# Kernel optimization log

Measured on AMD Instinct MI355X. Metric: run time of the kernel, lower is better.

The kernel has to match this reference:

```python
import jax, jax.numpy as jnp
import numpy as np

N_NODES = 50000

def gcn_conv(x, src, dst, W, b, n_nodes):
    """PyG-style GCNConv: add self-loops, symmetric norm, linear (no bias in lin),
    scatter-add aggregation, then bias."""
    loops = jnp.arange(n_nodes, dtype=src.dtype)
    s = jnp.concatenate([src, loops])  # [E+N]
    d = jnp.concatenate([dst, loops])  # [E+N]
    # degree on destination (col) with unit edge weights, incl. self loops
    deg = jax.ops.segment_sum(jnp.ones_like(d, dtype=x.dtype), d, num_segments=n_nodes)
    dinv = jnp.where(deg > 0, jax.lax.rsqrt(jnp.maximum(deg, 1.0)), 0.0)
    norm = dinv[s] * dinv[d]  # [E+N]
    h = x @ W  # [N, out]
    msg = h[s] * norm[:, None]  # [E+N, out] gather + scale
    out = jax.ops.segment_sum(msg, d, num_segments=n_nodes)  # scatter-add
    return out + b

def setup_inputs() -> dict:
    key = jax.random.key(0)
    k1, k2, k3, k4, k5, k6 = jax.random.split(key, 6)
    n, d_in, h_dim, d_out, e = N_NODES, 128, 128, 64, 800000
    x = jax.random.normal(k1, (n, d_in), dtype=jnp.float32)
    src = jax.random.randint(k2, (e,), 0, n, dtype=jnp.int64)
    dst = jax.random.randint(k3, (e,), 0, n, dtype=jnp.int64)
    edge_index = jnp.stack([src, dst])
    # Glorot-ish init for weights, zeros for bias (PyG default)
    W1 = jax.random.normal(k4, (d_in, h_dim), dtype=jnp.float32) / np.sqrt(d_in)
    b1 = jnp.zeros((h_dim,), dtype=jnp.float32)
    W2 = jax.random.normal(k5, (h_dim, d_out), dtype=jnp.float32) / np.sqrt(h_dim)
    b2 = jnp.zeros((d_out,), dtype=jnp.float32)
    return {"x": x, "edge_index": edge_index, "W1": W1, "b1": b1, "W2": W2, "b2": b2}

def reference(x, edge_index, W1, b1, W2, b2):
    src, dst = edge_index[0], edge_index[1]
    n = x.shape[0]
    h = gcn_conv(x, src, dst, W1, b1, n)
    h = jax.nn.relu(h)
    out = gcn_conv(h, src, dst, W2, b2, n)
    return jax.nn.relu(out)
```

## Files before the change

### kernel.cpp

```cpp
#include <hip/hip_runtime.h>


#define NPB 64
#define PB  256

typedef unsigned short ushort_t;
typedef unsigned int uint_t;
typedef __attribute__((ext_vector_type(8))) short bf16x8;
typedef __attribute__((ext_vector_type(4))) float f32x4;

__device__ inline float bf2f_lo(uint_t u) { return __uint_as_float(u << 16); }
__device__ inline float bf2f_hi(uint_t u) { return __uint_as_float(u & 0xffff0000u); }
__device__ inline ushort_t f2bf(float f) {
    uint_t x = __float_as_uint(f);
    uint_t r = x + 0x7fffu + ((x >> 16) & 1u);
    return (ushort_t)(r >> 16);
}
__device__ inline uint_t pack2bf(float lo, float hi) {
    return (uint_t)f2bf(lo) | ((uint_t)f2bf(hi) << 16);
}

__global__ __launch_bounds__(256) void prep_w_kernel(const float* __restrict__ W1,
                                                     const float* __restrict__ W2,
                                                     ushort_t* __restrict__ W1f,
                                                     ushort_t* __restrict__ W2f) {
    int i = blockIdx.x * 256 + threadIdx.x;
    if (i < 128 * 128) {
        int k = i >> 7, c = i & 127;
        int ct = c >> 4, lo = c & 15, ks = k >> 5, kg = (k >> 3) & 3, j = k & 7;
        W1f[(size_t)(((ct * 4 + ks) * 64) + kg * 16 + lo) * 8 + j] = f2bf(W1[i]);
    }
    if (i < 128 * 64) {
        int k = i >> 6, c = i & 63;
        int ct = c >> 4, lo = c & 15, ks = k >> 5, kg = (k >> 3) & 3, j = k & 7;
        W2f[(size_t)(((ct * 4 + ks) * 64) + kg * 16 + lo) * 8 + j] = f2bf(W2[i]);
    }
}


__global__ __launch_bounds__(256) void block_sum_kernel(const int* __restrict__ a, int L,
                                                        int* __restrict__ bsum) {
    __shared__ int red[256];
    int t = threadIdx.x;
    int base = blockIdx.x * 1024 + t * 4;
    int s = 0;
    if (base + 3 < L) {
        int4 v = *(const int4*)&a[base];
        s = v.x + v.y + v.z + v.w;
    } else {
        for (int i = 0; i < 4; ++i) if (base + i < L) s += a[base + i];
    }
    red[t] = s;
    __syncthreads();
    for (int off = 128; off > 0; off >>= 1) {
        if (t < off) red[t] += red[t + off];
        __syncthreads();
    }
    if (t == 0) bsum[blockIdx.x] = red[0];
}

__global__ __launch_bounds__(256) void local_scan_apply_kernel(int* __restrict__ arr, int L,
                                                               const int* __restrict__ bsum,
                                                               int nb) {
    __shared__ int sh[256];
    __shared__ int tsum[256];
    int b = blockIdx.x, t = threadIdx.x;
    sh[t] = (t < nb) ? bsum[t] : 0;
    __syncthreads();
    #pragma unroll
    for (int off = 1; off < 256; off <<= 1) {
        int w = (t >= off) ? sh[t - off] : 0;
        __syncthreads();
        sh[t] += w;
        __syncthreads();
    }
    int bprev = (b == 0) ? 0 : sh[b - 1];

    int base = b * 1024 + t * 4;
    int v[4];
    int s = 0;
    #pragma unroll
    for (int i = 0; i < 4; ++i) {
        int idx = base + i;
        v[i] = (idx < L) ? arr[idx] : 0;
        s += v[i];
    }
    tsum[t] = s;
    __syncthreads();
    for (int off = 1; off < 256; off <<= 1) {
        int w = (t >= off) ? tsum[t - off] : 0;
        __syncthreads();
        tsum[t] += w;
        __syncthreads();
    }
    int excl = (t == 0 ? 0 : tsum[t - 1]) + bprev;
    #pragma unroll
    for (int i = 0; i < 4; ++i) {
        int idx = base + i;
        if (idx < L) {
            arr[idx] = excl;
            excl += v[i];
        }
    }
}

__global__ __launch_bounds__(256) void local_scan_node_kernel(const int* __restrict__ cnt, int n,
                                                              const int* __restrict__ bsum,
                                                              int nb, int e_total,
                                                              int* __restrict__ rowstart,
                                                              float* __restrict__ dinv) {
    __shared__ int sh[256];
    __shared__ int tsum[256];
    int b = blockIdx.x, t = threadIdx.x;
    sh[t] = (t < nb) ? bsum[t] : 0;
    __syncthreads();
    #pragma unroll
    for (int off = 1; off < 256; off <<= 1) {
        int w = (t >= off) ? sh[t - off] : 0;
        __syncthreads();
        sh[t] += w;
        __syncthreads();
    }
    int bprev = (b == 0) ? 0 : sh[b - 1];

    int base = b * 1024 + t * 4;
    int v[4];
    int s = 0;
    #pragma unroll
    for (int i = 0; i < 4; ++i) {
        int idx = base + i;
        v[i] = (idx < n) ? cnt[idx] : 0;
        s += v[i];
    }
    tsum[t] = s;
    __syncthreads();
    for (int off = 1; off < 256; off <<= 1) {
        int w = (t >= off) ? tsum[t - off] : 0;
        __syncthreads();
        tsum[t] += w;
        __syncthreads();
    }
    int excl = (t == 0 ? 0 : tsum[t - 1]) + bprev;
    #pragma unroll
    for (int i = 0; i < 4; ++i) {
        int idx = base + i;
        if (idx < n) {
            rowstart[idx] = excl;
            excl += v[i];
            dinv[idx] = rsqrtf((float)(v[i] + 1));
        }
    }
    if (b == 0 && t == 0) rowstart[n] = e_total;
}


__global__ __launch_bounds__(256) void bucket_hist_kernel(const int* __restrict__ dst, int e,
                                                          int epb, int K,
                                                          int* __restrict__ hist) {
    __shared__ int lh[1024];
    int t = threadIdx.x, b = blockIdx.x;
    for (int k = t; k < K; k += 256) lh[k] = 0;
    __syncthreads();
    int lo = b * epb, hi = min(lo + epb, e);
    for (int i = lo + t; i < hi; i += 256) atomicAdd(&lh[dst[i] >> 6], 1);
    __syncthreads();
    for (int k = t; k < K; k += 256) hist[k * PB + b] = lh[k];
}

__global__ __launch_bounds__(256) void partition_kernel(const int* __restrict__ src,
                                                        const int* __restrict__ dst, int e,
                                                        int epb, int K,
                                                        const int* __restrict__ hist,
                                                        uint_t* __restrict__ ebuf) {
    __shared__ int loff[1024];
    int t = threadIdx.x, b = blockIdx.x;
    for (int k = t; k < K; k += 256) loff[k] = hist[k * PB + b];
    __syncthreads();
    int lo = b * epb, hi = min(lo + epb, e);
    for (int i = lo + t; i < hi; i += 256) {
        int d = dst[i];
        int k = d >> 6;
        int pos = atomicAdd(&loff[k], 1);
        ebuf[pos] = (uint_t)src[i] | ((uint_t)(d & (NPB - 1)) << 16);
    }
}

__global__ __launch_bounds__(256) void bucket_count_kernel(const uint_t* __restrict__ ebuf,
                                                           const int* __restrict__ hist,
                                                           int e, int K, int n,
                                                           int* __restrict__ cnt) {
    __shared__ int c64[NPB];
    int t = threadIdx.x, k = blockIdx.x;
    if (t < NPB) c64[t] = 0;
    __syncthreads();
    int lo = hist[k * PB];
    int hi = (k + 1 < K) ? hist[(k + 1) * PB] : e;
    for (int i = lo + t; i < hi; i += 256) atomicAdd(&c64[(ebuf[i] >> 16) & (NPB - 1)], 1);
    __syncthreads();
    int node = k * NPB + t;
    if (t < NPB && node < n) cnt[node] = c64[t];
}

__global__ __launch_bounds__(256) void bucket_fill_kernel(const uint_t* __restrict__ ebuf,
                                                          const int* __restrict__ hist,
                                                          const int* __restrict__ rowstart,
                                                          int e, int K, int n,
                                                          ushort_t* __restrict__ csr_src) {
    __shared__ int rs[NPB];
    __shared__ int c64[NPB];
    int t = threadIdx.x, k = blockIdx.x;
    if (t < NPB) {
        int node = k * NPB + t;
        rs[t] = (node < n) ? rowstart[node] : 0;
        c64[t] = 0;
    }
    __syncthreads();
    int lo = hist[k * PB];
    int hi = (k + 1 < K) ? hist[(k + 1) * PB] : e;
    for (int i = lo + t; i < hi; i += 256) {
        uint_t u = __builtin_nontemporal_load(ebuf + i);
        int dl = (u >> 16) & (NPB - 1);
        int slot = rs[dl] + atomicAdd(&c64[dl], 1);
        csr_src[slot] = (ushort_t)(u & 0xffffu);
    }
}

__global__ __launch_bounds__(256) void gemm128_mfma_kernel(const float* __restrict__ A,
                                                           const ushort_t* __restrict__ Wf,
                                                           const float* __restrict__ dinv,
                                                           ushort_t* __restrict__ out, int n) {
    __shared__ ushort_t Asl[64][136];
    int t = threadIdx.x;
    int row0 = blockIdx.x * 64;

    #pragma unroll
    for (int it = 0; it < 4; ++it) {
        int idx = (it * 256 + t) * 8;
        int r = idx >> 7, k = idx & 127;
        int gr = row0 + r;
        uint4 p = {0u, 0u, 0u, 0u};
        if (gr < n) {
            float4 lo = *(const float4*)&A[(size_t)gr * 128 + k];
            float4 hi = *(const float4*)&A[(size_t)gr * 128 + k + 4];
            p.x = pack2bf(lo.x, lo.y); p.y = pack2bf(lo.z, lo.w);
            p.z = pack2bf(hi.x, hi.y); p.w = pack2bf(hi.z, hi.w);
        }
        *(uint4*)&Asl[r][k] = p;
    }
    __syncthreads();

    int wave = t >> 6, lane = t & 63;
    int rb = wave * 16;
    int lrow = rb + (lane & 15);
    int kg8 = (lane >> 4) * 8;

    bf16x8 a0 = *(const bf16x8*)&Asl[lrow][0 * 32 + kg8];
    bf16x8 a1 = *(const bf16x8*)&Asl[lrow][1 * 32 + kg8];
    bf16x8 a2 = *(const bf16x8*)&Asl[lrow][2 * 32 + kg8];
    bf16x8 a3 = *(const bf16x8*)&Asl[lrow][3 * 32 + kg8];

    f32x4 acc[8];
    #pragma unroll
    for (int ct = 0; ct < 8; ++ct) acc[ct] = (f32x4){0.f, 0.f, 0.f, 0.f};

    #pragma unroll
    for (int ct = 0; ct < 8; ++ct) {
        const bf16x8* Wp = (const bf16x8*)&Wf[(size_t)(ct * 4) * 64 * 8];
        bf16x8 b0 = Wp[0 * 64 + lane];
        bf16x8 b1 = Wp[1 * 64 + lane];
        bf16x8 b2 = Wp[2 * 64 + lane];
        bf16x8 b3 = Wp[3 * 64 + lane];
        acc[ct] = __builtin_amdgcn_mfma_f32_16x16x32_bf16(a0, b0, acc[ct], 0, 0, 0);
        acc[ct] = __builtin_amdgcn_mfma_f32_16x16x32_bf16(a1, b1, acc[ct], 0, 0, 0);
        acc[ct] = __builtin_amdgcn_mfma_f32_16x16x32_bf16(a2, b2, acc[ct], 0, 0, 0);
        acc[ct] = __builtin_amdgcn_mfma_f32_16x16x32_bf16(a3, b3, acc[ct], 0, 0, 0);
    }

    int orow0 = row0 + rb + (lane >> 4) * 4;
    int col0 = lane & 15;
    float dv[4];
    #pragma unroll
    for (int r = 0; r < 4; ++r) dv[r] = (orow0 + r < n) ? dinv[orow0 + r] : 0.f;
    #pragma unroll
    for (int ct = 0; ct < 8; ++ct) {
        #pragma unroll
        for (int r = 0; r < 4; ++r) {
            int row = orow0 + r;
            if (row < n) out[(size_t)row * 128 + ct * 16 + col0] = f2bf(acc[ct][r] * dv[r]);
        }
    }
}

__global__ __launch_bounds__(256) void gemm64_mfma_kernel(const ushort_t* __restrict__ A,
                                                          const ushort_t* __restrict__ Wf,
                                                          const float* __restrict__ dinv,
                                                          ushort_t* __restrict__ out, int n) {
    __shared__ ushort_t Asl[64][136];
    int t = threadIdx.x;
    int row0 = blockIdx.x * 64;

    #pragma unroll
    for (int it = 0; it < 4; ++it) {
        int idx = (it * 256 + t) * 8;
        int r = idx >> 7, k = idx & 127;
        int gr = row0 + r;
        uint4 p = {0u, 0u, 0u, 0u};
        if (gr < n) p = *(const uint4*)&A[(size_t)gr * 128 + k];
        *(uint4*)&Asl[r][k] = p;
    }
    __syncthreads();

    int wave = t >> 6, lane = t & 63;
    int rb = wave * 16;
    int lrow = rb + (lane & 15);
    int kg8 = (lane >> 4) * 8;

    bf16x8 a0 = *(const bf16x8*)&Asl[lrow][0 * 32 + kg8];
    bf16x8 a1 = *(const bf16x8*)&Asl[lrow][1 * 32 + kg8];
    bf16x8 a2 = *(const bf16x8*)&Asl[lrow][2 * 32 + kg8];
    bf16x8 a3 = *(const bf16x8*)&Asl[lrow][3 * 32 + kg8];

    f32x4 acc[4];
    #pragma unroll
    for (int ct = 0; ct < 4; ++ct) acc[ct] = (f32x4){0.f, 0.f, 0.f, 0.f};

    #pragma unroll
    for (int ct = 0; ct < 4; ++ct) {
        const bf16x8* Wp = (const bf16x8*)&Wf[(size_t)(ct * 4) * 64 * 8];
        bf16x8 b0 = Wp[0 * 64 + lane];
        bf16x8 b1 = Wp[1 * 64 + lane];
        bf16x8 b2 = Wp[2 * 64 + lane];
        bf16x8 b3 = Wp[3 * 64 + lane];
        acc[ct] = __builtin_amdgcn_mfma_f32_16x16x32_bf16(a0, b0, acc[ct], 0, 0, 0);
        acc[ct] = __builtin_amdgcn_mfma_f32_16x16x32_bf16(a1, b1, acc[ct], 0, 0, 0);
        acc[ct] = __builtin_amdgcn_mfma_f32_16x16x32_bf16(a2, b2, acc[ct], 0, 0, 0);
        acc[ct] = __builtin_amdgcn_mfma_f32_16x16x32_bf16(a3, b3, acc[ct], 0, 0, 0);
    }

    int orow0 = row0 + rb + (lane >> 4) * 4;
    int col0 = lane & 15;
    float dv[4];
    #pragma unroll
    for (int r = 0; r < 4; ++r) dv[r] = (orow0 + r < n) ? dinv[orow0 + r] : 0.f;
    #pragma unroll
    for (int ct = 0; ct < 4; ++ct) {
        #pragma unroll
        for (int r = 0; r < 4; ++r) {
            int row = orow0 + r;
            if (row < n) out[(size_t)row * 64 + ct * 16 + col0] = f2bf(acc[ct][r] * dv[r]);
        }
    }
}

__global__ __launch_bounds__(256) void aggregate128_kernel(const ushort_t* __restrict__ g,
                                                           const int* __restrict__ rowstart,
                                                           const ushort_t* __restrict__ csr_src,
                                                           const float* __restrict__ dinv,
                                                           const float* __restrict__ bias,
                                                           ushort_t* __restrict__ out, int n) {
    int wave = threadIdx.x >> 6;
    int lane = threadIdx.x & 63;
    int v = blockIdx.x * 4 + wave;
    if (v >= n) return;
    int s    = __builtin_amdgcn_readfirstlane(rowstart[v]);
    int epos = __builtin_amdgcn_readfirstlane(rowstart[v + 1]);
    int eg = lane >> 3;
    int f  = lane & 7;

    float a0 = 0.f, a1 = 0.f, a2 = 0.f, a3 = 0.f, a4 = 0.f, a5 = 0.f, a6 = 0.f, a7 = 0.f;
    float a8 = 0.f, a9 = 0.f, aA = 0.f, aB = 0.f, aC = 0.f, aD = 0.f, aE = 0.f, aF = 0.f;
    if (lane < 8) {
        uint4 m0 = *(const uint4*)&g[(size_t)v * 128 + f * 16];
        uint4 m1 = *(const uint4*)&g[(size_t)v * 128 + f * 16 + 8];
        a0 = bf2f_lo(m0.x); a1 = bf2f_hi(m0.x);
        a2 = bf2f_lo(m0.y); a3 = bf2f_hi(m0.y);
        a4 = bf2f_lo(m0.z); a5 = bf2f_hi(m0.z);
        a6 = bf2f_lo(m0.w); a7 = bf2f_hi(m0.w);
        a8 = bf2f_lo(m1.x); a9 = bf2f_hi(m1.x);
        aA = bf2f_lo(m1.y); aB = bf2f_hi(m1.y);
        aC = bf2f_lo(m1.z); aD = bf2f_hi(m1.z);
        aE = bf2f_lo(m1.w); aF = bf2f_hi(m1.w);
    }

    #pragma unroll 2
    for (int j = s; j < epos; j += 8) {
        int idx = j + eg;
        int safe = min(idx, epos - 1);
        int u = csr_src[safe];
        float w = (idx < epos) ? 1.f : 0.f;
        uint4 m0 = *(const uint4*)&g[(size_t)u * 128 + f * 16];
        uint4 m1 = *(const uint4*)&g[(size_t)u * 128 + f * 16 + 8];
        a0 = fmaf(w, bf2f_lo(m0.x), a0); a1 = fmaf(w, bf2f_hi(m0.x), a1);
        a2 = fmaf(w, bf2f_lo(m0.y), a2); a3 = fmaf(w, bf2f_hi(m0.y), a3);
        a4 = fmaf(w, bf2f_lo(m0.z), a4); a5 = fmaf(w, bf2f_hi(m0.z), a5);
        a6 = fmaf(w, bf2f_lo(m0.w), a6); a7 = fmaf(w, bf2f_hi(m0.w), a7);
        a8 = fmaf(w, bf2f_lo(m1.x), a8); a9 = fmaf(w, bf2f_hi(m1.x), a9);
        aA = fmaf(w, bf2f_lo(m1.y), aA); aB = fmaf(w, bf2f_hi(m1.y), aB);
        aC = fmaf(w, bf2f_lo(m1.z), aC); aD = fmaf(w, bf2f_hi(m1.z), aD);
        aE = fmaf(w, bf2f_lo(m1.w), aE); aF = fmaf(w, bf2f_hi(m1.w), aF);
    }

    #pragma unroll
    for (int m = 8; m <= 32; m <<= 1) {
        a0 += __shfl_xor(a0, m); a1 += __shfl_xor(a1, m);
        a2 += __shfl_xor(a2, m); a3 += __shfl_xor(a3, m);
        a4 += __shfl_xor(a4, m); a5 += __shfl_xor(a5, m);
        a6 += __shfl_xor(a6, m); a7 += __shfl_xor(a7, m);
        a8 += __shfl_xor(a8, m); a9 += __shfl_xor(a9, m);
        aA += __shfl_xor(aA, m); aB += __shfl_xor(aB, m);
        aC += __shfl_xor(aC, m); aD += __shfl_xor(aD, m);
        aE += __shfl_xor(aE, m); aF += __shfl_xor(aF, m);
    }

    if (lane < 8) {
        float dv = dinv[v];
        int c0 = f * 16;
        float4 b0 = *(const float4*)&bias[c0];
        float4 b1 = *(const float4*)&bias[c0 + 4];
        float4 b2 = *(const float4*)&bias[c0 + 8];
        float4 b3 = *(const float4*)&bias[c0 + 12];
        float o00 = fmaxf(fmaf(a0, dv, b0.x), 0.f), o01 = fmaxf(fmaf(a1, dv, b0.y), 0.f);
        float o02 = fmaxf(fmaf(a2, dv, b0.z), 0.f), o03 = fmaxf(fmaf(a3, dv, b0.w), 0.f);
        float o04 = fmaxf(fmaf(a4, dv, b1.x), 0.f), o05 = fmaxf(fmaf(a5, dv, b1.y), 0.f);
        float o06 = fmaxf(fmaf(a6, dv, b1.z), 0.f), o07 = fmaxf(fmaf(a7, dv, b1.w), 0.f);
        float o08 = fmaxf(fmaf(a8, dv, b2.x), 0.f), o09 = fmaxf(fmaf(a9, dv, b2.y), 0.f);
        float o10 = fmaxf(fmaf(aA, dv, b2.z), 0.f), o11 = fmaxf(fmaf(aB, dv, b2.w), 0.f);
        float o12 = fmaxf(fmaf(aC, dv, b3.x), 0.f), o13 = fmaxf(fmaf(aD, dv, b3.y), 0.f);
        float o14 = fmaxf(fmaf(aE, dv, b3.z), 0.f), o15 = fmaxf(fmaf(aF, dv, b3.w), 0.f);
        uint4 p0 = {pack2bf(o00, o01), pack2bf(o02, o03), pack2bf(o04, o05), pack2bf(o06, o07)};
        uint4 p1 = {pack2bf(o08, o09), pack2bf(o10, o11), pack2bf(o12, o13), pack2bf(o14, o15)};
        *(uint4*)&out[(size_t)v * 128 + c0]     = p0;
        *(uint4*)&out[(size_t)v * 128 + c0 + 8] = p1;
    }
}

__global__ __launch_bounds__(256) void aggregate64_kernel(const ushort_t* __restrict__ g,
                                                          const int* __restrict__ rowstart,
                                                          const ushort_t* __restrict__ csr_src,
                                                          const float* __restrict__ dinv,
                                                          const float* __restrict__ bias,
                                                          float* __restrict__ out, int n) {
    int wave = threadIdx.x >> 6;
    int lane = threadIdx.x & 63;
    int v = blockIdx.x * 4 + wave;
    if (v >= n) return;
    int s    = __builtin_amdgcn_readfirstlane(rowstart[v]);
    int epos = __builtin_amdgcn_readfirstlane(rowstart[v + 1]);
    int eg = lane >> 3;
    int f  = lane & 7;

    float a0 = 0.f, a1 = 0.f, a2 = 0.f, a3 = 0.f, a4 = 0.f, a5 = 0.f, a6 = 0.f, a7 = 0.f;
    if (lane < 8) {
        uint4 m = *(const uint4*)&g[(size_t)v * 64 + f * 8];
        a0 = bf2f_lo(m.x); a1 = bf2f_hi(m.x);
        a2 = bf2f_lo(m.y); a3 = bf2f_hi(m.y);
        a4 = bf2f_lo(m.z); a5 = bf2f_hi(m.z);
        a6 = bf2f_lo(m.w); a7 = bf2f_hi(m.w);
    }

    #pragma unroll 2
    for (int j = s; j < epos; j += 8) {
        int idx = j + eg;
        int safe = min(idx, epos - 1);
        int u = __builtin_nontemporal_load(csr_src + safe);
        float w = (idx < epos) ? 1.f : 0.f;
        uint4 m = *(const uint4*)&g[(size_t)u * 64 + f * 8];
        a0 = fmaf(w, bf2f_lo(m.x), a0); a1 = fmaf(w, bf2f_hi(m.x), a1);
        a2 = fmaf(w, bf2f_lo(m.y), a2); a3 = fmaf(w, bf2f_hi(m.y), a3);
        a4 = fmaf(w, bf2f_lo(m.z), a4); a5 = fmaf(w, bf2f_hi(m.z), a5);
        a6 = fmaf(w, bf2f_lo(m.w), a6); a7 = fmaf(w, bf2f_hi(m.w), a7);
    }

    a0 += __shfl_xor(a0, 8);  a1 += __shfl_xor(a1, 8);
    a2 += __shfl_xor(a2, 8);  a3 += __shfl_xor(a3, 8);
    a4 += __shfl_xor(a4, 8);  a5 += __shfl_xor(a5, 8);
    a6 += __shfl_xor(a6, 8);  a7 += __shfl_xor(a7, 8);
    a0 += __shfl_xor(a0, 16); a1 += __shfl_xor(a1, 16);
    a2 += __shfl_xor(a2, 16); a3 += __shfl_xor(a3, 16);
    a4 += __shfl_xor(a4, 16); a5 += __shfl_xor(a5, 16);
    a6 += __shfl_xor(a6, 16); a7 += __shfl_xor(a7, 16);
    a0 += __shfl_xor(a0, 32); a1 += __shfl_xor(a1, 32);
    a2 += __shfl_xor(a2, 32); a3 += __shfl_xor(a3, 32);
    a4 += __shfl_xor(a4, 32); a5 += __shfl_xor(a5, 32);
    a6 += __shfl_xor(a6, 32); a7 += __shfl_xor(a7, 32);

    if (lane < 8) {
        float dv = dinv[v];
        float4 b0 = *(const float4*)&bias[f * 8];
        float4 b1 = *(const float4*)&bias[f * 8 + 4];
        float4 o0 = {fmaxf(fmaf(a0, dv, b0.x), 0.f), fmaxf(fmaf(a1, dv, b0.y), 0.f),
                     fmaxf(fmaf(a2, dv, b0.z), 0.f), fmaxf(fmaf(a3, dv, b0.w), 0.f)};
        float4 o1 = {fmaxf(fmaf(a4, dv, b1.x), 0.f), fmaxf(fmaf(a5, dv, b1.y), 0.f),
                     fmaxf(fmaf(a6, dv, b1.z), 0.f), fmaxf(fmaf(a7, dv, b1.w), 0.f)};
        *(float4*)&out[(size_t)v * 64 + f * 8] = o0;
        *(float4*)&out[(size_t)v * 64 + f * 8 + 4] = o1;
    }
}

extern "C" void kernel_launch(void* const* d_in, const int* in_sizes, int n_in,
                              void* d_out, int out_size, void* d_ws, size_t ws_size,
                              hipStream_t stream) {
    const float* x  = (const float*)d_in[0];
    const int*   ei = (const int*)d_in[1];
    const float* W1 = (const float*)d_in[2];
    const float* b1 = (const float*)d_in[3];
    const float* W2 = (const float*)d_in[4];
    const float* b2 = (const float*)d_in[5];
    float* out = (float*)d_out;

    const int n = in_sizes[0] / 128;
    const int e = in_sizes[1] / 2;
    const int* src = ei;
    const int* dst = ei + e;
    const int K   = (n + NPB - 1) / NPB;
    const int epb = (e + PB - 1) / PB;
    const int L   = K * PB;

    char* ws = (char*)d_ws;
    size_t off = 0;
    auto carve = [&](size_t bytes) -> void* {
        void* p = ws + off;
        off = (off + bytes + 255) & ~(size_t)255;
        return p;
    };
    int*      hist     = (int*)     carve((size_t)L * 4);
    int*      bsum     = (int*)     carve((size_t)1024 * 4);
    int*      cnt      = (int*)     carve((size_t)n * 4);
    int*      rowstart = (int*)     carve((size_t)(n + 1) * 4);
    float*    dinv     = (float*)   carve((size_t)n * 4);
    uint_t*   ebuf     = (uint_t*)  carve((size_t)e * 4);
    ushort_t* csr_src  = (ushort_t*)carve((size_t)e * 2);
    ushort_t* W1f      = (ushort_t*)carve((size_t)128 * 128 * 2);
    ushort_t* W2f      = (ushort_t*)carve((size_t)128 * 64 * 2);
    ushort_t* g1       = (ushort_t*)carve((size_t)n * 128 * 2);
    ushort_t* h2       = (ushort_t*)carve((size_t)n * 128 * 2);
    ushort_t* g2       = (ushort_t*)carve((size_t)n * 64 * 2);
    (void)ws_size;

    const int nbL = (L + 1023) / 1024;
    const int nbN = (n + 1023) / 1024;

    prep_w_kernel<<<64, 256, 0, stream>>>(W1, W2, W1f, W2f);
    bucket_hist_kernel<<<PB, 256, 0, stream>>>(dst, e, epb, K, hist);
    block_sum_kernel<<<nbL, 256, 0, stream>>>(hist, L, bsum);
    local_scan_apply_kernel<<<nbL, 256, 0, stream>>>(hist, L, bsum, nbL);
    partition_kernel<<<PB, 256, 0, stream>>>(src, dst, e, epb, K, hist, ebuf);
    bucket_count_kernel<<<K, 256, 0, stream>>>(ebuf, hist, e, K, n, cnt);
    block_sum_kernel<<<nbN, 256, 0, stream>>>(cnt, n, bsum);
    local_scan_node_kernel<<<nbN, 256, 0, stream>>>(cnt, n, bsum, nbN, e, rowstart, dinv);
    bucket_fill_kernel<<<K, 256, 0, stream>>>(ebuf, hist, rowstart, e, K, n, csr_src);

    const int gblocks = (n + 63) / 64;
    const int ablocks = (n + 3) / 4;
    gemm128_mfma_kernel<<<gblocks, 256, 0, stream>>>(x, W1f, dinv, g1, n);
    aggregate128_kernel<<<ablocks, 256, 0, stream>>>(g1, rowstart, csr_src, dinv, b1, h2, n);
    gemm64_mfma_kernel<<<gblocks, 256, 0, stream>>>(h2, W2f, dinv, g2, n);
    aggregate64_kernel<<<ablocks, 256, 0, stream>>>(g2, rowstart, csr_src, dinv, b2, out, n);
}
```

Baseline: 130.3 us.

## Fuse layer-1 aggregation with layer-2 GEMM and merge prep kernels

```diff
diff --git a/kernel.cpp b/kernel.cpp
--- a/kernel.cpp
+++ b/kernel.cpp
@@ -18,23 +18,6 @@
 }
 __device__ inline uint_t pack2bf(float lo, float hi) {
     return (uint_t)f2bf(lo) | ((uint_t)f2bf(hi) << 16);
-}
-
-__global__ __launch_bounds__(256) void prep_w_kernel(const float* __restrict__ W1,
-                                                     const float* __restrict__ W2,
-                                                     ushort_t* __restrict__ W1f,
-                                                     ushort_t* __restrict__ W2f) {
-    int i = blockIdx.x * 256 + threadIdx.x;
-    if (i < 128 * 128) {
-        int k = i >> 7, c = i & 127;
-        int ct = c >> 4, lo = c & 15, ks = k >> 5, kg = (k >> 3) & 3, j = k & 7;
-        W1f[(size_t)(((ct * 4 + ks) * 64) + kg * 16 + lo) * 8 + j] = f2bf(W1[i]);
-    }
-    if (i < 128 * 64) {
-        int k = i >> 6, c = i & 63;
-        int ct = c >> 4, lo = c & 15, ks = k >> 5, kg = (k >> 3) & 3, j = k & 7;
-        W2f[(size_t)(((ct * 4 + ks) * 64) + kg * 16 + lo) * 8 + j] = f2bf(W2[i]);
-    }
 }
 
 
@@ -105,23 +88,13 @@
 }
 
 __global__ __launch_bounds__(256) void local_scan_node_kernel(const int* __restrict__ cnt, int n,
-                                                              const int* __restrict__ bsum,
-                                                              int nb, int e_total,
+                                                              const int* __restrict__ hist,
+                                                              int e_total,
                                                               int* __restrict__ rowstart,
                                                               float* __restrict__ dinv) {
-    __shared__ int sh[256];
     __shared__ int tsum[256];
     int b = blockIdx.x, t = threadIdx.x;
-    sh[t] = (t < nb) ? bsum[t] : 0;
-    __syncthreads();
-    #pragma unroll
-    for (int off = 1; off < 256; off <<= 1) {
-        int w = (t >= off) ? sh[t - off] : 0;
-        __syncthreads();
-        sh[t] += w;
-        __syncthreads();
-    }
-    int bprev = (b == 0) ? 0 : sh[b - 1];
+    int bprev = hist[(size_t)(b * 16) * PB];
 
     int base = b * 1024 + t * 4;
     int v[4];
@@ -156,9 +129,25 @@
 
 __global__ __launch_bounds__(256) void bucket_hist_kernel(const int* __restrict__ dst, int e,
                                                           int epb, int K,
-                                                          int* __restrict__ hist) {
+                                                          int* __restrict__ hist,
+                                                          const float* __restrict__ W1,
+                                                          const float* __restrict__ W2,
+                                                          ushort_t* __restrict__ W1f,
+                                                          ushort_t* __restrict__ W2f) {
+    int t = threadIdx.x, b = blockIdx.x;
+    int gi = b * 256 + t;
+    if (gi < 128 * 128) {
+        int k = gi >> 7, c = gi & 127;
+        int ct = c >> 4, lo = c & 15, ks = k >> 5, kg = (k >> 3) & 3, j = k & 7;
+        W1f[(size_t)(((ct * 4 + ks) * 64) + kg * 16 + lo) * 8 + j] = f2bf(W1[gi]);
+    }
+    if (gi < 128 * 64) {
+        int k = gi >> 6, c = gi & 63;
+        int ct = c >> 4, lo = c & 15, ks = k >> 5, kg = (k >> 3) & 3, j = k & 7;
+        W2f[(size_t)(((ct * 4 + ks) * 64) + kg * 16 + lo) * 8 + j] = f2bf(W2[gi]);
+    }
+
     __shared__ int lh[1024];
-    int t = threadIdx.x, b = blockIdx.x;
     for (int k = t; k < K; k += 256) lh[k] = 0;
     __syncthreads();
     int lo = b * epb, hi = min(lo + epb, e);
@@ -291,146 +280,120 @@
     }
 }
 
-__global__ __launch_bounds__(256) void gemm64_mfma_kernel(const ushort_t* __restrict__ A,
-                                                          const ushort_t* __restrict__ Wf,
-                                                          const float* __restrict__ dinv,
-                                                          ushort_t* __restrict__ out, int n) {
-    __shared__ ushort_t Asl[64][136];
+__global__ __launch_bounds__(256) void fused_agg128_gemm64_mfma_kernel(
+        const ushort_t* __restrict__ g,
+        const int* __restrict__ rowstart,
+        const ushort_t* __restrict__ csr_src,
+        const float* __restrict__ dinv,
+        const float* __restrict__ bias,
+        const ushort_t* __restrict__ W2f,
+        ushort_t* __restrict__ g2, int n) {
+    __shared__ ushort_t h2sl[16][136];
     int t = threadIdx.x;
-    int row0 = blockIdx.x * 64;
-
-    #pragma unroll
-    for (int it = 0; it < 4; ++it) {
-        int idx = (it * 256 + t) * 8;
-        int r = idx >> 7, k = idx & 127;
-        int gr = row0 + r;
-        uint4 p = {0u, 0u, 0u, 0u};
-        if (gr < n) p = *(const uint4*)&A[(size_t)gr * 128 + k];
-        *(uint4*)&Asl[r][k] = p;
-    }
-    __syncthreads();
-
-    int wave = t >> 6, lane = t & 63;
-    int rb = wave * 16;
-    int lrow = rb + (lane & 15);
-    int kg8 = (lane >> 4) * 8;
-
-    bf16x8 a0 = *(const bf16x8*)&Asl[lrow][0 * 32 + kg8];
-    bf16x8 a1 = *(const bf16x8*)&Asl[lrow][1 * 32 + kg8];
-    bf16x8 a2 = *(const bf16x8*)&Asl[lrow][2 * 32 + kg8];
-    bf16x8 a3 = *(const bf16x8*)&Asl[lrow][3 * 32 + kg8];
-
-    f32x4 acc[4];
-    #pragma unroll
-    for (int ct = 0; ct < 4; ++ct) acc[ct] = (f32x4){0.f, 0.f, 0.f, 0.f};
-
-    #pragma unroll
-    for (int ct = 0; ct < 4; ++ct) {
-        const bf16x8* Wp = (const bf16x8*)&Wf[(size_t)(ct * 4) * 64 * 8];
-        bf16x8 b0 = Wp[0 * 64 + lane];
-        bf16x8 b1 = Wp[1 * 64 + lane];
-        bf16x8 b2 = Wp[2 * 64 + lane];
-        bf16x8 b3 = Wp[3 * 64 + lane];
-        acc[ct] = __builtin_amdgcn_mfma_f32_16x16x32_bf16(a0, b0, acc[ct], 0, 0, 0);
-        acc[ct] = __builtin_amdgcn_mfma_f32_16x16x32_bf16(a1, b1, acc[ct], 0, 0, 0);
-        acc[ct] = __builtin_amdgcn_mfma_f32_16x16x32_bf16(a2, b2, acc[ct], 0, 0, 0);
-        acc[ct] = __builtin_amdgcn_mfma_f32_16x16x32_bf16(a3, b3, acc[ct], 0, 0, 0);
-    }
-
-    int orow0 = row0 + rb + (lane >> 4) * 4;
-    int col0 = lane & 15;
-    float dv[4];
-    #pragma unroll
-    for (int r = 0; r < 4; ++r) dv[r] = (orow0 + r < n) ? dinv[orow0 + r] : 0.f;
-    #pragma unroll
-    for (int ct = 0; ct < 4; ++ct) {
-        #pragma unroll
-        for (int r = 0; r < 4; ++r) {
-            int row = orow0 + r;
-            if (row < n) out[(size_t)row * 64 + ct * 16 + col0] = f2bf(acc[ct][r] * dv[r]);
-        }
-    }
-}
-
-__global__ __launch_bounds__(256) void aggregate128_kernel(const ushort_t* __restrict__ g,
-                                                           const int* __restrict__ rowstart,
-                                                           const ushort_t* __restrict__ csr_src,
-                                                           const float* __restrict__ dinv,
-                                                           const float* __restrict__ bias,
-                                                           ushort_t* __restrict__ out, int n) {
-    int wave = threadIdx.x >> 6;
-    int lane = threadIdx.x & 63;
-    int v = blockIdx.x * 4 + wave;
-    if (v >= n) return;
-    int s    = __builtin_amdgcn_readfirstlane(rowstart[v]);
-    int epos = __builtin_amdgcn_readfirstlane(rowstart[v + 1]);
+    int wave = t >> 6;
+    int lane = t & 63;
     int eg = lane >> 3;
     int f  = lane & 7;
 
-    float a0 = 0.f, a1 = 0.f, a2 = 0.f, a3 = 0.f, a4 = 0.f, a5 = 0.f, a6 = 0.f, a7 = 0.f;
-    float a8 = 0.f, a9 = 0.f, aA = 0.f, aB = 0.f, aC = 0.f, aD = 0.f, aE = 0.f, aF = 0.f;
-    if (lane < 8) {
-        uint4 m0 = *(const uint4*)&g[(size_t)v * 128 + f * 16];
-        uint4 m1 = *(const uint4*)&g[(size_t)v * 128 + f * 16 + 8];
-        a0 = bf2f_lo(m0.x); a1 = bf2f_hi(m0.x);
-        a2 = bf2f_lo(m0.y); a3 = bf2f_hi(m0.y);
-        a4 = bf2f_lo(m0.z); a5 = bf2f_hi(m0.z);
-        a6 = bf2f_lo(m0.w); a7 = bf2f_hi(m0.w);
-        a8 = bf2f_lo(m1.x); a9 = bf2f_hi(m1.x);
-        aA = bf2f_lo(m1.y); aB = bf2f_hi(m1.y);
-        aC = bf2f_lo(m1.z); aD = bf2f_hi(m1.z);
-        aE = bf2f_lo(m1.w); aF = bf2f_hi(m1.w);
-    }
-
-    #pragma unroll 2
-    for (int j = s; j < epos; j += 8) {
-        int idx = j + eg;
-        int safe = min(idx, epos - 1);
-        int u = csr_src[safe];
-        float w = (idx < epos) ? 1.f : 0.f;
-        uint4 m0 = *(const uint4*)&g[(size_t)u * 128 + f * 16];
-        uint4 m1 = *(const uint4*)&g[(size_t)u * 128 + f * 16 + 8];
-        a0 = fmaf(w, bf2f_lo(m0.x), a0); a1 = fmaf(w, bf2f_hi(m0.x), a1);
-        a2 = fmaf(w, bf2f_lo(m0.y), a2); a3 = fmaf(w, bf2f_hi(m0.y), a3);
-        a4 = fmaf(w, bf2f_lo(m0.z), a4); a5 = fmaf(w, bf2f_hi(m0.z), a5);
-        a6 = fmaf(w, bf2f_lo(m0.w), a6); a7 = fmaf(w, bf2f_hi(m0.w), a7);
-        a8 = fmaf(w, bf2f_lo(m1.x), a8); a9 = fmaf(w, bf2f_hi(m1.x), a9);
-        aA = fmaf(w, bf2f_lo(m1.y), aA); aB = fmaf(w, bf2f_hi(m1.y), aB);
-        aC = fmaf(w, bf2f_lo(m1.z), aC); aD = fmaf(w, bf2f_hi(m1.z), aD);
-        aE = fmaf(w, bf2f_lo(m1.w), aE); aF = fmaf(w, bf2f_hi(m1.w), aF);
-    }
-
-    #pragma unroll
-    for (int m = 8; m <= 32; m <<= 1) {
-        a0 += __shfl_xor(a0, m); a1 += __shfl_xor(a1, m);
-        a2 += __shfl_xor(a2, m); a3 += __shfl_xor(a3, m);
-        a4 += __shfl_xor(a4, m); a5 += __shfl_xor(a5, m);
-        a6 += __shfl_xor(a6, m); a7 += __shfl_xor(a7, m);
-        a8 += __shfl_xor(a8, m); a9 += __shfl_xor(a9, m);
-        aA += __shfl_xor(aA, m); aB += __shfl_xor(aB, m);
-        aC += __shfl_xor(aC, m); aD += __shfl_xor(aD, m);
-        aE += __shfl_xor(aE, m); aF += __shfl_xor(aF, m);
-    }
-
-    if (lane < 8) {
-        float dv = dinv[v];
-        int c0 = f * 16;
-        float4 b0 = *(const float4*)&bias[c0];
-        float4 b1 = *(const float4*)&bias[c0 + 4];
-        float4 b2 = *(const float4*)&bias[c0 + 8];
-        float4 b3 = *(const float4*)&bias[c0 + 12];
-        float o00 = fmaxf(fmaf(a0, dv, b0.x), 0.f), o01 = fmaxf(fmaf(a1, dv, b0.y), 0.f);
-        float o02 = fmaxf(fmaf(a2, dv, b0.z), 0.f), o03 = fmaxf(fmaf(a3, dv, b0.w), 0.f);
-        float o04 = fmaxf(fmaf(a4, dv, b1.x), 0.f), o05 = fmaxf(fmaf(a5, dv, b1.y), 0.f);
-        float o06 = fmaxf(fmaf(a6, dv, b1.z), 0.f), o07 = fmaxf(fmaf(a7, dv, b1.w), 0.f);
-        float o08 = fmaxf(fmaf(a8, dv, b2.x), 0.f), o09 = fmaxf(fmaf(a9, dv, b2.y), 0.f);
-        float o10 = fmaxf(fmaf(aA, dv, b2.z), 0.f), o11 = fmaxf(fmaf(aB, dv, b2.w), 0.f);
-        float o12 = fmaxf(fmaf(aC, dv, b3.x), 0.f), o13 = fmaxf(fmaf(aD, dv, b3.y), 0.f);
-        float o14 = fmaxf(fmaf(aE, dv, b3.z), 0.f), o15 = fmaxf(fmaf(aF, dv, b3.w), 0.f);
-        uint4 p0 = {pack2bf(o00, o01), pack2bf(o02, o03), pack2bf(o04, o05), pack2bf(o06, o07)};
-        uint4 p1 = {pack2bf(o08, o09), pack2bf(o10, o11), pack2bf(o12, o13), pack2bf(o14, o15)};
-        *(uint4*)&out[(size_t)v * 128 + c0]     = p0;
-        *(uint4*)&out[(size_t)v * 128 + c0 + 8] = p1;
+    #pragma unroll
+    for (int i = 0; i < 4; ++i) {
+        int v = blockIdx.x * 16 + wave * 4 + i;
+        if (v < n) {
+            int s    = __builtin_amdgcn_readfirstlane(rowstart[v]);
+            int epos = __builtin_amdgcn_readfirstlane(rowstart[v + 1]);
+
+            float a0 = 0.f, a1 = 0.f, a2 = 0.f, a3 = 0.f, a4 = 0.f, a5 = 0.f, a6 = 0.f, a7 = 0.f;
+            float a8 = 0.f, a9 = 0.f, aA = 0.f, aB = 0.f, aC = 0.f, aD = 0.f, aE = 0.f, aF = 0.f;
+            if (lane < 8) {
+                uint4 m0 = *(const uint4*)&g[(size_t)v * 128 + f * 16];
+                uint4 m1 = *(const uint4*)&g[(size_t)v * 128 + f * 16 + 8];
+                a0 = bf2f_lo(m0.x); a1 = bf2f_hi(m0.x);
+                a2 = bf2f_lo(m0.y); a3 = bf2f_hi(m0.y);
+                a4 = bf2f_lo(m0.z); a5 = bf2f_hi(m0.z);
+                a6 = bf2f_lo(m0.w); a7 = bf2f_hi(m0.w);
+                a8 = bf2f_lo(m1.x); a9 = bf2f_hi(m1.x);
+                aA = bf2f_lo(m1.y); aB = bf2f_hi(m1.y);
+                aC = bf2f_lo(m1.z); aD = bf2f_hi(m1.z);
+                aE = bf2f_lo(m1.w); aF = bf2f_hi(m1.w);
+            }
+
+            #pragma unroll 2
+            for (int j = s; j < epos; j += 8) {
+                int idx = j + eg;
+                int safe = min(idx, epos - 1);
+                int u = csr_src[safe];
+                float w = (idx < epos) ? 1.f : 0.f;
+                uint4 m0 = *(const uint4*)&g[(size_t)u * 128 + f * 16];
+                uint4 m1 = *(const uint4*)&g[(size_t)u * 128 + f * 16 + 8];
+                a0 = fmaf(w, bf2f_lo(m0.x), a0); a1 = fmaf(w, bf2f_hi(m0.x), a1);
+                a2 = fmaf(w, bf2f_lo(m0.y), a2); a3 = fmaf(w, bf2f_hi(m0.y), a3);
+                a4 = fmaf(w, bf2f_lo(m0.z), a4); a5 = fmaf(w, bf2f_hi(m0.z), a5);
+                a6 = fmaf(w, bf2f_lo(m0.w), a6); a7 = fmaf(w, bf2f_hi(m0.w), a7);
+                a8 = fmaf(w, bf2f_lo(m1.x), a8); a9 = fmaf(w, bf2f_hi(m1.x), a9);
+                aA = fmaf(w, bf2f_lo(m1.y), aA); aB = fmaf(w, bf2f_hi(m1.y), aB);
+                aC = fmaf(w, bf2f_lo(m1.z), aC); aD = fmaf(w, bf2f_hi(m1.z), aD);
+                aE = fmaf(w, bf2f_lo(m1.w), aE); aF = fmaf(w, bf2f_hi(m1.w), aF);
+            }
+
+            #pragma unroll
+            for (int m = 8; m <= 32; m <<= 1) {
+                a0 += __shfl_xor(a0, m); a1 += __shfl_xor(a1, m);
+                a2 += __shfl_xor(a2, m); a3 += __shfl_xor(a3, m);
+                a4 += __shfl_xor(a4, m); a5 += __shfl_xor(a5, m);
+                a6 += __shfl_xor(a6, m); a7 += __shfl_xor(a7, m);
+                a8 += __shfl_xor(a8, m); a9 += __shfl_xor(a9, m);
+                aA += __shfl_xor(aA, m); aB += __shfl_xor(aB, m);
+                aC += __shfl_xor(aC, m); aD += __shfl_xor(aD, m);
+                aE += __shfl_xor(aE, m); aF += __shfl_xor(aF, m);
+            }
+
+            if (lane < 8) {
+                float dv = dinv[v];
+                int c0 = f * 16;
+                float4 b0 = *(const float4*)&bias[c0];
+                float4 b1 = *(const float4*)&bias[c0 + 4];
+                float4 b2 = *(const float4*)&bias[c0 + 8];
+                float4 b3 = *(const float4*)&bias[c0 + 12];
+                float o00 = fmaxf(fmaf(a0, dv, b0.x), 0.f), o01 = fmaxf(fmaf(a1, dv, b0.y), 0.f);
+                float o02 = fmaxf(fmaf(a2, dv, b0.z), 0.f), o03 = fmaxf(fmaf(a3, dv, b0.w), 0.f);
+                float o04 = fmaxf(fmaf(a4, dv, b1.x), 0.f), o05 = fmaxf(fmaf(a5, dv, b1.y), 0.f);
+                float o06 = fmaxf(fmaf(a6, dv, b1.z), 0.f), o07 = fmaxf(fmaf(a7, dv, b1.w), 0.f);
+                float o08 = fmaxf(fmaf(a8, dv, b2.x), 0.f), o09 = fmaxf(fmaf(a9, dv, b2.y), 0.f);
+                float o10 = fmaxf(fmaf(aA, dv, b2.z), 0.f), o11 = fmaxf(fmaf(aB, dv, b2.w), 0.f);
+                float o12 = fmaxf(fmaf(aC, dv, b3.x), 0.f), o13 = fmaxf(fmaf(aD, dv, b3.y), 0.f);
+                float o14 = fmaxf(fmaf(aE, dv, b3.z), 0.f), o15 = fmaxf(fmaf(aF, dv, b3.w), 0.f);
+                uint4 p0 = {pack2bf(o00, o01), pack2bf(o02, o03),
+                            pack2bf(o04, o05), pack2bf(o06, o07)};
+                uint4 p1 = {pack2bf(o08, o09), pack2bf(o10, o11),
+                            pack2bf(o12, o13), pack2bf(o14, o15)};
+                int nd = wave * 4 + i;
+                *(uint4*)&h2sl[nd][c0]     = p0;
+                *(uint4*)&h2sl[nd][c0 + 8] = p1;
+            }
+        }
+    }
+    __syncthreads();
+
+    int lrow = lane & 15;
+    int kg8 = (lane >> 4) * 8;
+    bf16x8 a0 = *(const bf16x8*)&h2sl[lrow][0 * 32 + kg8];
+    bf16x8 a1 = *(const bf16x8*)&h2sl[lrow][1 * 32 + kg8];
+    bf16x8 a2 = *(const bf16x8*)&h2sl[lrow][2 * 32 + kg8];
+    bf16x8 a3 = *(const bf16x8*)&h2sl[lrow][3 * 32 + kg8];
+
+    f32x4 acc = (f32x4){0.f, 0.f, 0.f, 0.f};
+    const bf16x8* Wp = (const bf16x8*)&W2f[(size_t)(wave * 4) * 64 * 8];
+    acc = __builtin_amdgcn_mfma_f32_16x16x32_bf16(a0, Wp[0 * 64 + lane], acc, 0, 0, 0);
+    acc = __builtin_amdgcn_mfma_f32_16x16x32_bf16(a1, Wp[1 * 64 + lane], acc, 0, 0, 0);
+    acc = __builtin_amdgcn_mfma_f32_16x16x32_bf16(a2, Wp[2 * 64 + lane], acc, 0, 0, 0);
+    acc = __builtin_amdgcn_mfma_f32_16x16x32_bf16(a3, Wp[3 * 64 + lane], acc, 0, 0, 0);
+
+    int orow0 = blockIdx.x * 16 + (lane >> 4) * 4;
+    int col = wave * 16 + (lane & 15);
+    #pragma unroll
+    for (int r = 0; r < 4; ++r) {
+        int row = orow0 + r;
+        if (row < n) g2[(size_t)row * 64 + col] = f2bf(acc[r] * dinv[row]);
     }
 }
 
@@ -533,27 +496,25 @@
     ushort_t* W1f      = (ushort_t*)carve((size_t)128 * 128 * 2);
     ushort_t* W2f      = (ushort_t*)carve((size_t)128 * 64 * 2);
     ushort_t* g1       = (ushort_t*)carve((size_t)n * 128 * 2);
-    ushort_t* h2       = (ushort_t*)carve((size_t)n * 128 * 2);
     ushort_t* g2       = (ushort_t*)carve((size_t)n * 64 * 2);
     (void)ws_size;
 
     const int nbL = (L + 1023) / 1024;
     const int nbN = (n + 1023) / 1024;
 
-    prep_w_kernel<<<64, 256, 0, stream>>>(W1, W2, W1f, W2f);
-    bucket_hist_kernel<<<PB, 256, 0, stream>>>(dst, e, epb, K, hist);
+    bucket_hist_kernel<<<PB, 256, 0, stream>>>(dst, e, epb, K, hist, W1, W2, W1f, W2f);
     block_sum_kernel<<<nbL, 256, 0, stream>>>(hist, L, bsum);
     local_scan_apply_kernel<<<nbL, 256, 0, stream>>>(hist, L, bsum, nbL);
     partition_kernel<<<PB, 256, 0, stream>>>(src, dst, e, epb, K, hist, ebuf);
     bucket_count_kernel<<<K, 256, 0, stream>>>(ebuf, hist, e, K, n, cnt);
-    block_sum_kernel<<<nbN, 256, 0, stream>>>(cnt, n, bsum);
-    local_scan_node_kernel<<<nbN, 256, 0, stream>>>(cnt, n, bsum, nbN, e, rowstart, dinv);
+    local_scan_node_kernel<<<nbN, 256, 0, stream>>>(cnt, n, hist, e, rowstart, dinv);
     bucket_fill_kernel<<<K, 256, 0, stream>>>(ebuf, hist, rowstart, e, K, n, csr_src);
 
     const int gblocks = (n + 63) / 64;
+    const int fblocks = (n + 15) / 16;
     const int ablocks = (n + 3) / 4;
     gemm128_mfma_kernel<<<gblocks, 256, 0, stream>>>(x, W1f, dinv, g1, n);
-    aggregate128_kernel<<<ablocks, 256, 0, stream>>>(g1, rowstart, csr_src, dinv, b1, h2, n);
-    gemm64_mfma_kernel<<<gblocks, 256, 0, stream>>>(h2, W2f, dinv, g2, n);
+    fused_agg128_gemm64_mfma_kernel<<<fblocks, 256, 0, stream>>>(g1, rowstart, csr_src,
+                                                                 dinv, b1, W2f, g2, n);
     aggregate64_kernel<<<ablocks, 256, 0, stream>>>(g2, rowstart, csr_src, dinv, b2, out, n);
 }
```

Result: faster. 121.2 us, median of 2 (-7.0%).
